# Optimization experiments

Measured on AMD Instinct MI355X. Metric: run time of the kernel, lower is better.

The kernel has to match this reference:

```python
import jax, jax.numpy as jnp
import numpy as np

N_NODES = 131072
IN_F = 512
HID = 512
H = 8
DH = HID // H
B = 1024  # batch_size (num graphs); static for jit
LN_EPS = 1e-5


def setup_inputs() -> dict:
    key = jax.random.key(0)
    ks = jax.random.split(key, 12)
    # equal-size segments (128 nodes/graph), sorted as in PyG batching
    batch = (jnp.arange(N_NODES) // (N_NODES // B)).astype(jnp.int32)
    s = 0.02
    return {
        "x": jax.random.normal(ks[0], (N_NODES, IN_F), jnp.float32),
        "batch": batch,
        "query": jax.random.normal(ks[1], (H, DH), jnp.float32) * s,
        "key_w": jax.random.normal(ks[2], (HID, IN_F), jnp.float32) * s,
        "key_b": jnp.zeros((HID,), jnp.float32),
        "value_w": jax.random.normal(ks[3], (HID, IN_F), jnp.float32) * s,
        "value_b": jnp.zeros((HID,), jnp.float32),
        "out_w": jax.random.normal(ks[4], (IN_F, HID), jnp.float32) * s,
        "out_b": jnp.zeros((IN_F,), jnp.float32),
        "gate_w": jax.random.normal(ks[5], (IN_F, 2 * IN_F), jnp.float32) * s,
        "gate_b": jnp.zeros((IN_F,), jnp.float32),
        "ln_w": jnp.ones((IN_F,), jnp.float32),
        "ln_b": jnp.zeros((IN_F,), jnp.float32),
    }


def reference(x, batch, query, key_w, key_b, value_w, value_b, out_w, out_b,
              gate_w, gate_b, ln_w, ln_b):
    N = x.shape[0]
    # projections (dense GEMMs)
    keys = (x @ key_w.T + key_b).reshape(N, H, DH)
    values = (x @ value_w.T + value_b).reshape(N, H, DH)
    # per-node attention logits against shared per-head query: [N, H]
    scores = jnp.einsum('nhd,hd->nh', keys, query)
    # segment softmax over nodes within each graph
    smax = jax.ops.segment_max(scores, batch, num_segments=B)  # [B, H]
    smax = jnp.where(jnp.isfinite(smax), smax, 0.0)            # guard empty graphs
    e = jnp.exp(scores - smax[batch])
    ssum = jax.ops.segment_sum(e, batch, num_segments=B)       # [B, H]
    w = e / jnp.maximum(ssum[batch], 1e-12)                    # [N, H]  (dropout is eval-mode identity)
    # attention-weighted pooling of values: [B, H, DH] -> [B, HID]
    pooled = jax.ops.segment_sum(w[:, :, None] * values, batch, num_segments=B)
    ctx = pooled.reshape(B, HID) @ out_w.T + out_b             # [B, IN_F]
    # gating with per-graph mean pool
    counts = jax.ops.segment_sum(jnp.ones((N,), x.dtype), batch, num_segments=B)
    avg = jax.ops.segment_sum(x, batch, num_segments=B) / jnp.maximum(counts, 1.0)[:, None]
    gate = jax.nn.sigmoid(jnp.concatenate([ctx, avg], axis=1) @ gate_w.T + gate_b)
    ctx = gate * ctx + (1.0 - gate) * avg
    emb = jnp.where(counts[:, None] > 0, ctx, 0.0)             # empty graphs stay zero
    # LayerNorm
    mu = emb.mean(-1, keepdims=True)
    var = emb.var(-1, keepdims=True)
    return (emb - mu) / jnp.sqrt(var + LN_EPS) * ln_w + ln_b
```

## Files before the change

### kernel.cpp

```cpp
#include <hip/hip_runtime.h>
#include <hip/hip_bf16.h>

typedef short short8 __attribute__((ext_vector_type(8)));
typedef float f32x4 __attribute__((ext_vector_type(4)));

#define NGRAPH 1024
#define NPG    128
#define INF    512
#define NHEAD  8
#define CH     32

__device__ __forceinline__ ushort f2b(float f){
  __hip_bfloat16 h(f);
  union { __hip_bfloat16 h; ushort u; } v; v.h = h; return v.u;
}
__device__ __forceinline__ float b2f_lo(unsigned u){
  union { unsigned u; float f; } v; v.u = u << 16; return v.f;
}
__device__ __forceinline__ float b2f_hi(unsigned u){
  union { unsigned u; float f; } v; v.u = u & 0xffff0000u; return v.f;
}

__global__ void k_kq(const float* __restrict__ q, const float* __restrict__ kw,
                     float* __restrict__ kq){
  int h = blockIdx.x, t = threadIdx.x;
  float s = 0.f;
  #pragma unroll 8
  for(int d = 0; d < 64; d++)
    s += q[h*64 + d] * kw[(size_t)(h*64 + d)*INF + t];
  kq[h*INF + t] = s;
}

__global__ __launch_bounds__(128, 2) void k_graph(
    const float* __restrict__ x, const float* __restrict__ kq,
    ushort* __restrict__ xw_b, float* __restrict__ avg_f, ushort* __restrict__ avg_b){
  __shared__ __align__(16) ushort xs[CH*INF];
  __shared__ __align__(16) float  sc[CH*NHEAD];
  __shared__ float mEf[3*NHEAD];

  const int t = threadIdx.x, lane = t & 63, w = t >> 6;
  const int col = lane & 15, kg = lane >> 4;
  const int g = blockIdx.x;
  const int node = w*16 + col;

  short8 bfrag[16];
  {
    const bool ok = (col < 8);
    const float* kqr = kq + col*INF;
    #pragma unroll
    for(int ks = 0; ks < 16; ks++){
      short8 v = short8{0,0,0,0,0,0,0,0};
      if(ok){
        float4 p0 = *(const float4*)(kqr + ks*32 + kg*8);
        float4 p1 = *(const float4*)(kqr + ks*32 + kg*8 + 4);
        v[0]=(short)f2b(p0.x); v[1]=(short)f2b(p0.y); v[2]=(short)f2b(p0.z); v[3]=(short)f2b(p0.w);
        v[4]=(short)f2b(p1.x); v[5]=(short)f2b(p1.y); v[6]=(short)f2b(p1.z); v[7]=(short)f2b(p1.w);
      }
      bfrag[ks] = v;
    }
  }

  if(t < NHEAD){ mEf[t] = -1e30f; mEf[NHEAD + t] = 0.f; }

  float acc[NHEAD][4];
  #pragma unroll
  for(int h = 0; h < NHEAD; h++)
    #pragma unroll
    for(int j = 0; j < 4; j++) acc[h][j] = 0.f;
  float cs[4] = {0.f, 0.f, 0.f, 0.f};

  for(int c = 0; c < 4; c++){
    {
      const float* xr = x + (size_t)(g*NPG + c*CH + node)*INF + kg*8;
      f32x4 sacc = {0.f,0.f,0.f,0.f};
      #pragma unroll
      for(int ks = 0; ks < 16; ks++){
        float4 a = *(const float4*)(xr + ks*32);
        float4 b = *(const float4*)(xr + ks*32 + 4);
        short8 af;
        af[0]=(short)f2b(a.x); af[1]=(short)f2b(a.y); af[2]=(short)f2b(a.z); af[3]=(short)f2b(a.w);
        af[4]=(short)f2b(b.x); af[5]=(short)f2b(b.y); af[6]=(short)f2b(b.z); af[7]=(short)f2b(b.w);
        *(short8*)((char*)xs + node*1024 + ((ks*64 + kg*16) ^ ((node & 7) << 4))) = af;
        sacc = __builtin_amdgcn_mfma_f32_16x16x32_bf16(af, bfrag[ks], sacc, 0, 0, 0);
      }
      if(col < 8){
        #pragma unroll
        for(int r = 0; r < 4; r++)
          sc[(w*16 + kg*4 + r)*NHEAD + col] = sacc[r];
      }
    }
    __syncthreads();

    {
      int h = t >> 4, s = t & 15;
      float v[2]; float m = -1e30f;
      #pragma unroll
      for(int i = 0; i < 2; i++){ v[i] = sc[(s + 16*i)*NHEAD + h]; m = fmaxf(m, v[i]); }
      #pragma unroll
      for(int msk = 1; msk < 16; msk <<= 1) m = fmaxf(m, __shfl_xor(m, msk));
      float es = 0.f;
      #pragma unroll
      for(int i = 0; i < 2; i++){ v[i] = __expf(v[i] - m); es += v[i]; }
      #pragma unroll
      for(int msk = 1; msk < 16; msk <<= 1) es += __shfl_xor(es, msk);
      float M = mEf[h], E = mEf[NHEAD + h];
      float Mn = fmaxf(M, m);
      float f_old = __expf(M - Mn), f_new = __expf(m - Mn);
      #pragma unroll
      for(int i = 0; i < 2; i++) sc[(s + 16*i)*NHEAD + h] = v[i]*f_new;
      if(s == 0){
        mEf[h] = Mn;
        mEf[NHEAD + h] = E*f_old + es*f_new;
        mEf[2*NHEAD + h] = f_old;
      }
    }
    __syncthreads();

    {
      float fo[NHEAD];
      #pragma unroll
      for(int h = 0; h < NHEAD; h++) fo[h] = mEf[2*NHEAD + h];
      #pragma unroll
      for(int h = 0; h < NHEAD; h++)
        #pragma unroll
        for(int j = 0; j < 4; j++) acc[h][j] *= fo[h];
      #pragma unroll 4
      for(int n = 0; n < CH; n++){
        uint2 xv = *(const uint2*)((const char*)xs + n*1024 + ((8*t) ^ ((n & 7) << 4)));
        float x0 = b2f_lo(xv.x), x1 = b2f_hi(xv.x);
        float x2 = b2f_lo(xv.y), x3 = b2f_hi(xv.y);
        float4 w0 = *(float4*)(sc + n*NHEAD);
        float4 w1 = *(float4*)(sc + n*NHEAD + 4);
        float wv[8] = {w0.x, w0.y, w0.z, w0.w, w1.x, w1.y, w1.z, w1.w};
        #pragma unroll
        for(int h = 0; h < NHEAD; h++){
          acc[h][0] += wv[h]*x0; acc[h][1] += wv[h]*x1;
          acc[h][2] += wv[h]*x2; acc[h][3] += wv[h]*x3;
        }
        cs[0] += x0; cs[1] += x1; cs[2] += x2; cs[3] += x3;
      }
    }
    __syncthreads();
  }

  #pragma unroll
  for(int h = 0; h < NHEAD; h++){
    float einv = 1.0f / fmaxf(mEf[NHEAD + h], 1e-12f);
    float v0 = acc[h][0]*einv, v1 = acc[h][1]*einv;
    float v2 = acc[h][2]*einv, v3 = acc[h][3]*einv;
    uint2 pk = { (unsigned)f2b(v0) | ((unsigned)f2b(v1) << 16),
                 (unsigned)f2b(v2) | ((unsigned)f2b(v3) << 16) };
    *(uint2*)(xw_b + (size_t)g*4096 + h*INF + 4*t) = pk;
  }
  float am0 = cs[0]*(1.0f/128.0f), am1 = cs[1]*(1.0f/128.0f);
  float am2 = cs[2]*(1.0f/128.0f), am3 = cs[3]*(1.0f/128.0f);
  float4 av = {am0, am1, am2, am3};
  *(float4*)(avg_f + (size_t)g*INF + 4*t) = av;
  uint2 pk = { (unsigned)f2b(am0) | ((unsigned)f2b(am1) << 16),
               (unsigned)f2b(am2) | ((unsigned)f2b(am3) << 16) };
  *(uint2*)(avg_b + (size_t)g*INF + 4*t) = pk;
}

__global__ __launch_bounds__(256, 4) void gemm_tn(
    const ushort* __restrict__ A1, const ushort* __restrict__ A2,
    int lda, int headmode,
    const float* __restrict__ Wt, int ldw,
    const float* __restrict__ bias,
    float* __restrict__ Cf, ushort* __restrict__ Cb,
    int ldc, int K, int ksplit){
  __shared__ ushort As[2][32*72];
  __shared__ ushort Bs[2][64*72];
  const int t = threadIdx.x, lane = t & 63, w = t >> 6;
  const int m0 = blockIdx.x*32, n0 = blockIdx.y*64;
  const int aoff = headmode ? blockIdx.y*512 : 0;
  const int col = lane & 15, kg = lane >> 4;
  const int ar = t >> 3, ak = (t & 7)*8;
  const int br = t >> 2, bk = (t & 3)*16;

  f32x4 acc[2];
  acc[0] = f32x4{0.f,0.f,0.f,0.f};
  acc[1] = f32x4{0.f,0.f,0.f,0.f};

  const ushort* Ap0 = (0 < ksplit) ? A1 : A2;
  short8 va = *(const short8*)(Ap0 + (size_t)(m0 + ar)*lda + aoff + ak);
  float4 wb0 = *(const float4*)(Wt + (size_t)(n0 + br)*ldw + bk);
  float4 wb1 = *(const float4*)(Wt + (size_t)(n0 + br)*ldw + bk + 4);
  float4 wb2 = *(const float4*)(Wt + (size_t)(n0 + br)*ldw + bk + 8);
  float4 wb3 = *(const float4*)(Wt + (size_t)(n0 + br)*ldw + bk + 12);
  int buf = 0;
  for(int kc = 0; kc < K; kc += 64){
    *(short8*)((char*)&As[buf][0] + ar*144 + ak*2) = va;
    {
      short8 b0, b1;
      b0[0]=(short)f2b(wb0.x); b0[1]=(short)f2b(wb0.y); b0[2]=(short)f2b(wb0.z); b0[3]=(short)f2b(wb0.w);
      b0[4]=(short)f2b(wb1.x); b0[5]=(short)f2b(wb1.y); b0[6]=(short)f2b(wb1.z); b0[7]=(short)f2b(wb1.w);
      b1[0]=(short)f2b(wb2.x); b1[1]=(short)f2b(wb2.y); b1[2]=(short)f2b(wb2.z); b1[3]=(short)f2b(wb2.w);
      b1[4]=(short)f2b(wb3.x); b1[5]=(short)f2b(wb3.y); b1[6]=(short)f2b(wb3.z); b1[7]=(short)f2b(wb3.w);
      *(short8*)((char*)&Bs[buf][0] + br*144 + bk*2)      = b0;
      *(short8*)((char*)&Bs[buf][0] + br*144 + bk*2 + 16) = b1;
    }
    __syncthreads();
    if(kc + 64 < K){
      int kn = kc + 64;
      const ushort* Ap = (kn < ksplit) ? A1 : A2;
      int kl = (kn < ksplit) ? kn : kn - ksplit;
      va  = *(const short8*)(Ap + (size_t)(m0 + ar)*lda + aoff + kl + ak);
      wb0 = *(const float4*)(Wt + (size_t)(n0 + br)*ldw + kn + bk);
      wb1 = *(const float4*)(Wt + (size_t)(n0 + br)*ldw + kn + bk + 4);
      wb2 = *(const float4*)(Wt + (size_t)(n0 + br)*ldw + kn + bk + 8);
      wb3 = *(const float4*)(Wt + (size_t)(n0 + br)*ldw + kn + bk + 12);
    }
    const int mr = (w & 1)*16, nc = (w >> 1)*32;
    #pragma unroll
    for(int kk = 0; kk < 2; kk++){
      short8 af  = *(short8*)((char*)&As[buf][0] + (mr + col)*144      + kk*64 + kg*16);
      short8 bf0 = *(short8*)((char*)&Bs[buf][0] + (nc + col)*144      + kk*64 + kg*16);
      short8 bf1 = *(short8*)((char*)&Bs[buf][0] + (nc + 16 + col)*144 + kk*64 + kg*16);
      acc[0] = __builtin_amdgcn_mfma_f32_16x16x32_bf16(af, bf0, acc[0], 0,0,0);
      acc[1] = __builtin_amdgcn_mfma_f32_16x16x32_bf16(af, bf1, acc[1], 0,0,0);
    }
    buf ^= 1;
  }
  #pragma unroll
  for(int ni = 0; ni < 2; ni++)
    #pragma unroll
    for(int r = 0; r < 4; r++){
      int rr = m0 + (w & 1)*16 + kg*4 + r;
      int cc = n0 + (w >> 1)*32 + ni*16 + col;
      float vv = acc[ni][r] + bias[cc];
      if(Cf) Cf[(size_t)rr*ldc + cc] = vv;
      if(Cb) Cb[(size_t)rr*ldc + cc] = f2b(vv);
    }
}

__global__ __launch_bounds__(512, 2) void k5_epilogue(
    const float* __restrict__ z, const float* __restrict__ ctx,
    const float* __restrict__ avg, const float* __restrict__ lnw,
    const float* __restrict__ lnb, float* __restrict__ out){
  __shared__ float red[16];
  const int t = threadIdx.x, b = blockIdx.x;
  const size_t i = (size_t)b*INF + t;
  float zz = z[i], c = ctx[i], a = avg[i];
  float g = 1.0f / (1.0f + __expf(-zz));
  float e = g*c + (1.0f - g)*a;
  float s1 = e, s2 = e*e;
  #pragma unroll
  for(int m = 1; m < 64; m <<= 1){ s1 += __shfl_xor(s1, m); s2 += __shfl_xor(s2, m); }
  int wv = t >> 6;
  if((t & 63) == 0){ red[wv] = s1; red[8 + wv] = s2; }
  __syncthreads();
  float ts1 = 0.f, ts2 = 0.f;
  #pragma unroll
  for(int k = 0; k < 8; k++){ ts1 += red[k]; ts2 += red[8 + k]; }
  float mu = ts1 * (1.0f/512.0f);
  float var = ts2 * (1.0f/512.0f) - mu*mu;
  out[i] = (e - mu) * rsqrtf(var + 1e-5f) * lnw[t] + lnb[t];
}

extern "C" void kernel_launch(void* const* d_in, const int* in_sizes, int n_in,
                              void* d_out, int out_size, void* d_ws, size_t ws_size,
                              hipStream_t stream){
  const float* x       = (const float*)d_in[0];
  const float* query   = (const float*)d_in[2];
  const float* key_w   = (const float*)d_in[3];
  const float* value_w = (const float*)d_in[5];
  const float* value_b = (const float*)d_in[6];
  const float* out_w   = (const float*)d_in[7];
  const float* out_b   = (const float*)d_in[8];
  const float* gate_w  = (const float*)d_in[9];
  const float* gate_b  = (const float*)d_in[10];
  const float* ln_w    = (const float*)d_in[11];
  const float* ln_b    = (const float*)d_in[12];
  float* out = (float*)d_out;

  char* ws = (char*)d_ws;
  float*  kq       = (float*) (ws + 0);
  ushort* xw_b     = (ushort*)(ws + 16384);
  float*  avg_f    = (float*) (ws + 8404992);
  ushort* avg_b    = (ushort*)(ws + 10502144);
  ushort* pooled_b = (ushort*)(ws + 11550720);
  float*  ctx_f    = (float*) (ws + 12599296);
  ushort* ctx_b    = (ushort*)(ws + 14696448);
  float*  z_f      = (float*) (ws + 15745024);

  k_kq<<<8, 512, 0, stream>>>(query, key_w, kq);

  k_graph<<<NGRAPH, 128, 0, stream>>>(x, kq, xw_b, avg_f, avg_b);

  gemm_tn<<<dim3(32, 8), 256, 0, stream>>>(xw_b, xw_b, 4096, 1, value_w, 512, value_b,
                                           nullptr, pooled_b, 512, 512, 1 << 30);
  gemm_tn<<<dim3(32, 8), 256, 0, stream>>>(pooled_b, pooled_b, 512, 0, out_w, 512, out_b,
                                           ctx_f, ctx_b, 512, 512, 1 << 30);
  gemm_tn<<<dim3(32, 8), 256, 0, stream>>>(ctx_b, avg_b, 512, 0, gate_w, 1024, gate_b,
                                           z_f, nullptr, 512, 1024, 512);

  k5_epilogue<<<NGRAPH, 512, 0, stream>>>(z_f, ctx_f, avg_f, ln_w, ln_b, out);
}
```

Measured before the change: 99.42 us.

## Pre-convert GEMM weights to bf16 in graph kernel and reshape GEMM tiles

The graph kernel now also converts value_w, out_w and gate_w from fp32 to bf16 into workspace, with each block converting a 1024-element slice. The small GEMMs then read bf16 weights directly, which removes the per-tile fp32 loads and conversions. Their tile shape changes from 32x64 to 64x32 to match, and the grid changes from 32x8 to 16x16. The extra conversion work in the graph kernel is small, but it adds a serial dependency and uses workspace.

```diff
diff --git a/kernel.cpp b/kernel.cpp
--- a/kernel.cpp
+++ b/kernel.cpp
@@ -33,6 +33,9 @@
 
 __global__ __launch_bounds__(128, 2) void k_graph(
     const float* __restrict__ x, const float* __restrict__ kq,
+    const float* __restrict__ vw, const float* __restrict__ ow,
+    const float* __restrict__ gw,
+    ushort* __restrict__ vwb, ushort* __restrict__ owb, ushort* __restrict__ gwb,
     ushort* __restrict__ xw_b, float* __restrict__ avg_f, ushort* __restrict__ avg_b){
   __shared__ __align__(16) ushort xs[CH*INF];
   __shared__ __align__(16) float  sc[CH*NHEAD];
@@ -42,6 +45,20 @@
   const int col = lane & 15, kg = lane >> 4;
   const int g = blockIdx.x;
   const int node = w*16 + col;
+
+  {
+    int idx = g*1024 + t*8;
+    const float* src; ushort* dst; int off;
+    if(idx < 262144){ src = vw; dst = vwb; off = idx; }
+    else if(idx < 524288){ src = ow; dst = owb; off = idx - 262144; }
+    else { src = gw; dst = gwb; off = idx - 524288; }
+    float4 a = *(const float4*)(src + off);
+    float4 b = *(const float4*)(src + off + 4);
+    short8 v;
+    v[0]=(short)f2b(a.x); v[1]=(short)f2b(a.y); v[2]=(short)f2b(a.z); v[3]=(short)f2b(a.w);
+    v[4]=(short)f2b(b.x); v[5]=(short)f2b(b.y); v[6]=(short)f2b(b.z); v[7]=(short)f2b(b.w);
+    *(short8*)(dst + off) = v;
+  }
 
   short8 bfrag[16];
   {
@@ -164,70 +181,59 @@
 __global__ __launch_bounds__(256, 4) void gemm_tn(
     const ushort* __restrict__ A1, const ushort* __restrict__ A2,
     int lda, int headmode,
-    const float* __restrict__ Wt, int ldw,
+    const ushort* __restrict__ Wt, int ldw,
     const float* __restrict__ bias,
     float* __restrict__ Cf, ushort* __restrict__ Cb,
     int ldc, int K, int ksplit){
-  __shared__ ushort As[2][32*72];
-  __shared__ ushort Bs[2][64*72];
+  __shared__ ushort As[2][64*72];
+  __shared__ ushort Bs[2][32*72];
   const int t = threadIdx.x, lane = t & 63, w = t >> 6;
-  const int m0 = blockIdx.x*32, n0 = blockIdx.y*64;
-  const int aoff = headmode ? blockIdx.y*512 : 0;
+  const int m0 = blockIdx.x*64, n0 = blockIdx.y*32;
+  const int aoff = headmode ? (blockIdx.y >> 1)*512 : 0;
   const int col = lane & 15, kg = lane >> 4;
-  const int ar = t >> 3, ak = (t & 7)*8;
-  const int br = t >> 2, bk = (t & 3)*16;
+  const int ar = t >> 2, ak = (t & 3)*16;
+  const int br = t >> 3, bk = (t & 7)*8;
 
   f32x4 acc[2];
   acc[0] = f32x4{0.f,0.f,0.f,0.f};
   acc[1] = f32x4{0.f,0.f,0.f,0.f};
 
   const ushort* Ap0 = (0 < ksplit) ? A1 : A2;
-  short8 va = *(const short8*)(Ap0 + (size_t)(m0 + ar)*lda + aoff + ak);
-  float4 wb0 = *(const float4*)(Wt + (size_t)(n0 + br)*ldw + bk);
-  float4 wb1 = *(const float4*)(Wt + (size_t)(n0 + br)*ldw + bk + 4);
-  float4 wb2 = *(const float4*)(Wt + (size_t)(n0 + br)*ldw + bk + 8);
-  float4 wb3 = *(const float4*)(Wt + (size_t)(n0 + br)*ldw + bk + 12);
+  short8 va0 = *(const short8*)(Ap0 + (size_t)(m0 + ar)*lda + aoff + ak);
+  short8 va1 = *(const short8*)(Ap0 + (size_t)(m0 + ar)*lda + aoff + ak + 8);
+  short8 vb  = *(const short8*)(Wt + (size_t)(n0 + br)*ldw + bk);
   int buf = 0;
   for(int kc = 0; kc < K; kc += 64){
-    *(short8*)((char*)&As[buf][0] + ar*144 + ak*2) = va;
-    {
-      short8 b0, b1;
-      b0[0]=(short)f2b(wb0.x); b0[1]=(short)f2b(wb0.y); b0[2]=(short)f2b(wb0.z); b0[3]=(short)f2b(wb0.w);
-      b0[4]=(short)f2b(wb1.x); b0[5]=(short)f2b(wb1.y); b0[6]=(short)f2b(wb1.z); b0[7]=(short)f2b(wb1.w);
-      b1[0]=(short)f2b(wb2.x); b1[1]=(short)f2b(wb2.y); b1[2]=(short)f2b(wb2.z); b1[3]=(short)f2b(wb2.w);
-      b1[4]=(short)f2b(wb3.x); b1[5]=(short)f2b(wb3.y); b1[6]=(short)f2b(wb3.z); b1[7]=(short)f2b(wb3.w);
-      *(short8*)((char*)&Bs[buf][0] + br*144 + bk*2)      = b0;
-      *(short8*)((char*)&Bs[buf][0] + br*144 + bk*2 + 16) = b1;
-    }
+    *(short8*)((char*)&As[buf][0] + ar*144 + ak*2)      = va0;
+    *(short8*)((char*)&As[buf][0] + ar*144 + ak*2 + 16) = va1;
+    *(short8*)((char*)&Bs[buf][0] + br*144 + bk*2)      = vb;
     __syncthreads();
     if(kc + 64 < K){
       int kn = kc + 64;
       const ushort* Ap = (kn < ksplit) ? A1 : A2;
       int kl = (kn < ksplit) ? kn : kn - ksplit;
-      va  = *(const short8*)(Ap + (size_t)(m0 + ar)*lda + aoff + kl + ak);
-      wb0 = *(const float4*)(Wt + (size_t)(n0 + br)*ldw + kn + bk);
-      wb1 = *(const float4*)(Wt + (size_t)(n0 + br)*ldw + kn + bk + 4);
-      wb2 = *(const float4*)(Wt + (size_t)(n0 + br)*ldw + kn + bk + 8);
-      wb3 = *(const float4*)(Wt + (size_t)(n0 + br)*ldw + kn + bk + 12);
-    }
-    const int mr = (w & 1)*16, nc = (w >> 1)*32;
+      va0 = *(const short8*)(Ap + (size_t)(m0 + ar)*lda + aoff + kl + ak);
+      va1 = *(const short8*)(Ap + (size_t)(m0 + ar)*lda + aoff + kl + ak + 8);
+      vb  = *(const short8*)(Wt + (size_t)(n0 + br)*ldw + kn + bk);
+    }
+    const int mr = (w & 1)*32, nc = (w >> 1)*16;
     #pragma unroll
     for(int kk = 0; kk < 2; kk++){
-      short8 af  = *(short8*)((char*)&As[buf][0] + (mr + col)*144      + kk*64 + kg*16);
-      short8 bf0 = *(short8*)((char*)&Bs[buf][0] + (nc + col)*144      + kk*64 + kg*16);
-      short8 bf1 = *(short8*)((char*)&Bs[buf][0] + (nc + 16 + col)*144 + kk*64 + kg*16);
-      acc[0] = __builtin_amdgcn_mfma_f32_16x16x32_bf16(af, bf0, acc[0], 0,0,0);
-      acc[1] = __builtin_amdgcn_mfma_f32_16x16x32_bf16(af, bf1, acc[1], 0,0,0);
+      short8 af0 = *(short8*)((char*)&As[buf][0] + (mr + col)*144      + kk*64 + kg*16);
+      short8 af1 = *(short8*)((char*)&As[buf][0] + (mr + 16 + col)*144 + kk*64 + kg*16);
+      short8 bf  = *(short8*)((char*)&Bs[buf][0] + (nc + col)*144      + kk*64 + kg*16);
+      acc[0] = __builtin_amdgcn_mfma_f32_16x16x32_bf16(af0, bf, acc[0], 0,0,0);
+      acc[1] = __builtin_amdgcn_mfma_f32_16x16x32_bf16(af1, bf, acc[1], 0,0,0);
     }
     buf ^= 1;
   }
   #pragma unroll
-  for(int ni = 0; ni < 2; ni++)
+  for(int mi = 0; mi < 2; mi++)
     #pragma unroll
     for(int r = 0; r < 4; r++){
-      int rr = m0 + (w & 1)*16 + kg*4 + r;
-      int cc = n0 + (w >> 1)*32 + ni*16 + col;
-      float vv = acc[ni][r] + bias[cc];
+      int rr = m0 + (w & 1)*32 + mi*16 + kg*4 + r;
+      int cc = n0 + (w >> 1)*16 + col;
+      float vv = acc[mi][r] + bias[cc];
       if(Cf) Cf[(size_t)rr*ldc + cc] = vv;
       if(Cb) Cb[(size_t)rr*ldc + cc] = f2b(vv);
     }
@@ -275,24 +281,28 @@
 
   char* ws = (char*)d_ws;
   float*  kq       = (float*) (ws + 0);
-  ushort* xw_b     = (ushort*)(ws + 16384);
-  float*  avg_f    = (float*) (ws + 8404992);
-  ushort* avg_b    = (ushort*)(ws + 10502144);
-  ushort* pooled_b = (ushort*)(ws + 11550720);
-  float*  ctx_f    = (float*) (ws + 12599296);
-  ushort* ctx_b    = (ushort*)(ws + 14696448);
-  float*  z_f      = (float*) (ws + 15745024);
+  ushort* vw_b     = (ushort*)(ws + 16384);
+  ushort* ow_b     = (ushort*)(ws + 540672);
+  ushort* gw_b     = (ushort*)(ws + 1064960);
+  ushort* xw_b     = (ushort*)(ws + 2113536);
+  float*  avg_f    = (float*) (ws + 10502144);
+  ushort* avg_b    = (ushort*)(ws + 12599296);
+  ushort* pooled_b = (ushort*)(ws + 13647872);
+  float*  ctx_f    = (float*) (ws + 14696448);
+  ushort* ctx_b    = (ushort*)(ws + 16793600);
+  float*  z_f      = (float*) (ws + 17842176);
 
   k_kq<<<8, 512, 0, stream>>>(query, key_w, kq);
 
-  k_graph<<<NGRAPH, 128, 0, stream>>>(x, kq, xw_b, avg_f, avg_b);
-
-  gemm_tn<<<dim3(32, 8), 256, 0, stream>>>(xw_b, xw_b, 4096, 1, value_w, 512, value_b,
-                                           nullptr, pooled_b, 512, 512, 1 << 30);
-  gemm_tn<<<dim3(32, 8), 256, 0, stream>>>(pooled_b, pooled_b, 512, 0, out_w, 512, out_b,
-                                           ctx_f, ctx_b, 512, 512, 1 << 30);
-  gemm_tn<<<dim3(32, 8), 256, 0, stream>>>(ctx_b, avg_b, 512, 0, gate_w, 1024, gate_b,
-                                           z_f, nullptr, 512, 1024, 512);
+  k_graph<<<NGRAPH, 128, 0, stream>>>(x, kq, value_w, out_w, gate_w,
+                                      vw_b, ow_b, gw_b, xw_b, avg_f, avg_b);
+
+  gemm_tn<<<dim3(16, 16), 256, 0, stream>>>(xw_b, xw_b, 4096, 1, vw_b, 512, value_b,
+                                            nullptr, pooled_b, 512, 512, 1 << 30);
+  gemm_tn<<<dim3(16, 16), 256, 0, stream>>>(pooled_b, pooled_b, 512, 0, ow_b, 512, out_b,
+                                            ctx_f, ctx_b, 512, 512, 1 << 30);
+  gemm_tn<<<dim3(16, 16), 256, 0, stream>>>(ctx_b, avg_b, 512, 0, gw_b, 1024, gate_b,
+                                            z_f, nullptr, 512, 1024, 512);
 
   k5_epilogue<<<NGRAPH, 512, 0, stream>>>(z_f, ctx_f, avg_f, ln_w, ln_b, out);
 }
```

After: 95.34 us. -4.1%, faster.
